# Kernel tuning notes

Measured on AMD Instinct MI355X. Metric: run time of the kernel, lower is better.

## Reference

```python
import jax, jax.numpy as jnp
import numpy as np
import math

B, T, IN_DIM = 4, 1024, 64
D, H, L, DFF = 1024, 16, 4, 4096
N_STEPS = 24
MAXLEN = 2048
DK = D // H


def _pos_encoding(max_len, d):
    pos = np.arange(max_len, dtype=np.float32)[:, None]
    div = np.exp(np.arange(0, d, 2, dtype=np.float32) * (-math.log(10000.0) / d))
    pe = np.zeros((max_len, d), dtype=np.float32)
    pe[:, 0::2] = np.sin(pos * div)
    pe[:, 1::2] = np.cos(pos * div)
    return jnp.asarray(pe)

_PE = _pos_encoding(MAXLEN, D)


def _lin(x, W, b):
    # torch Linear convention: W is (out, in)
    return x @ W.T + b


def _mha(q, kv, Wq, bq, Wk, bk, Wv, bv, Wo, bo):
    Bq, Tq, _ = q.shape
    Tk = kv.shape[1]
    Qh = _lin(q, Wq, bq).reshape(Bq, Tq, H, DK).transpose(0, 2, 1, 3)
    Kh = _lin(kv, Wk, bk).reshape(Bq, Tk, H, DK).transpose(0, 2, 1, 3)
    Vh = _lin(kv, Wv, bv).reshape(Bq, Tk, H, DK).transpose(0, 2, 1, 3)
    scores = jnp.einsum('bhqd,bhkd->bhqk', Qh, Kh) / math.sqrt(DK)
    probs = jax.nn.softmax(scores, axis=-1)
    out = jnp.einsum('bhqk,bhkd->bhqd', probs, Vh)
    out = out.transpose(0, 2, 1, 3).reshape(Bq, Tq, D)
    return _lin(out, Wo, bo)


def _ffn(x, W1, b1, W2, b2):
    return _lin(jax.nn.relu(_lin(x, W1, b1)), W2, b2)


def _ln(x, g, b, eps=1e-5):
    mu = jnp.mean(x, axis=-1, keepdims=True)
    var = jnp.var(x, axis=-1, keepdims=True)
    return (x - mu) / jnp.sqrt(var + eps) * g + b


def setup_inputs() -> dict:
    key = jax.random.key(0)
    ks = iter(jax.random.split(key, 64))
    def w(shape, s=0.02):
        return jax.random.normal(next(ks), shape, jnp.float32) * s
    inp = {'x': jax.random.normal(next(ks), (B, T, IN_DIM), jnp.float32)}
    inp['in_W'] = w((D, IN_DIM)); inp['in_b'] = jnp.zeros((D,), jnp.float32)
    for p in ['enc', 'dec']:
        for n in ['Wq', 'Wk', 'Wv', 'Wo']:
            inp[f'{p}_{n}'] = w((L, D, D))
            inp[f'{p}_b{n[1].lower()}'] = jnp.zeros((L, D), jnp.float32)
    for p in ['ffe', 'ffd']:
        inp[f'{p}_W1'] = w((DFF, D)); inp[f'{p}_b1'] = jnp.zeros((DFF,), jnp.float32)
        inp[f'{p}_W2'] = w((D, DFF)); inp[f'{p}_b2'] = jnp.zeros((D,), jnp.float32)
    for p in ['ne', 'nd']:
        inp[f'{p}_g'] = jnp.ones((D,), jnp.float32); inp[f'{p}_b'] = jnp.zeros((D,), jnp.float32)
    inp['out_W'] = w((1, D)); inp['out_b'] = jnp.zeros((1,), jnp.float32)
    inp['temb_W'] = w((D, 1)); inp['temb_b'] = jnp.zeros((D,), jnp.float32)
    return inp


def reference(x, in_W, in_b,
              enc_Wq, enc_bq, enc_Wk, enc_bk, enc_Wv, enc_bv, enc_Wo, enc_bo,
              ffe_W1, ffe_b1, ffe_W2, ffe_b2, ne_g, ne_b,
              dec_Wq, dec_bq, dec_Wk, dec_bk, dec_Wv, dec_bv, dec_Wo, dec_bo,
              ffd_W1, ffd_b1, ffd_W2, ffd_b2, nd_g, nd_b,
              out_W, out_b, temb_W, temb_b):
    batch, seq, _ = x.shape
    h = _lin(x, in_W, in_b) + _PE[:seq]
    for l in range(L):
        h = _mha(h, h, enc_Wq[l], enc_bq[l], enc_Wk[l], enc_bk[l],
                 enc_Wv[l], enc_bv[l], enc_Wo[l], enc_bo[l])
        h = _ln(h + _ffn(h, ffe_W1, ffe_b1, ffe_W2, ffe_b2), ne_g, ne_b)
    dec = jnp.zeros((batch, 1, D), x.dtype)
    preds = []
    for _ in range(N_STEPS):
        d = dec + _PE[:dec.shape[1]]
        for l in range(L):
            # same layer weights used for self- and cross-attention, as in source
            d = _mha(d, d, dec_Wq[l], dec_bq[l], dec_Wk[l], dec_bk[l],
                     dec_Wv[l], dec_bv[l], dec_Wo[l], dec_bo[l])
            d = _mha(d, h, dec_Wq[l], dec_bq[l], dec_Wk[l], dec_bk[l],
                     dec_Wv[l], dec_bv[l], dec_Wo[l], dec_bo[l])
            d = _ln(d + _ffn(d, ffd_W1, ffd_b1, ffd_W2, ffd_b2), nd_g, nd_b)
        step = _lin(d[:, -1, :], out_W, out_b)        # (B, 1)
        preds.append(step[:, None, :])                 # (B, 1, 1)
        emb = _lin(step, temb_W, temb_b)[:, None, :]   # (B, 1, D)
        dec = jnp.concatenate([dec, emb], axis=1)
    return jnp.concatenate(preds, axis=1)              # (B, n_steps, 1)
```

## Files before the change

kernel.cpp:

```cpp
#include <hip/hip_runtime.h>
#include <math.h>

#define DM    1024
#define NH    16
#define DKH   64
#define NL    4
#define DFFN  4096
#define BB    4
#define TT    1024
#define NSTEP 24
#define BT    (BB*TT)
#define MD    (BB*NSTEP)
#define CSPLIT 8
#define CKEYS  (TT/CSPLIT)
#define PSTRIDE ((size_t)MD*DM)
#define PSTRIDE_F ((size_t)MD*DFFN)

typedef __attribute__((ext_vector_type(8))) short s16x8;
typedef __attribute__((ext_vector_type(4))) short s16x4;
typedef __attribute__((ext_vector_type(4))) float f32x4;

__device__ inline short f2b(float f){
  unsigned u = __float_as_uint(f);
  u += 0x7fffu + ((u>>16)&1u);
  return (short)(u>>16);
}
__device__ inline float b2f(short h){
  return __uint_as_float(((unsigned)(unsigned short)h)<<16);
}

__device__ inline float wave_sum(float v){
  #pragma unroll
  for (int off=1; off<64; off<<=1) v += __shfl_xor(v, off, 64);
  return v;
}

__global__ __launch_bounds__(256)
void split_kernel(const float* __restrict__ X, short* __restrict__ Hi,
                  short* __restrict__ Lo, int n8)
{
  const size_t i = (size_t)blockIdx.x*256 + threadIdx.x;
  if (i >= (size_t)n8) return;
  const float4 v0 = *(const float4*)(X + i*8);
  const float4 v1 = *(const float4*)(X + i*8 + 4);
  const float f[8] = {v0.x,v0.y,v0.z,v0.w,v1.x,v1.y,v1.z,v1.w};
  s16x8 hv, lv;
  #pragma unroll
  for (int e=0;e<8;e++){
    const short h = f2b(f[e]);
    hv[e] = h;
    lv[e] = f2b(f[e] - b2f(h));
  }
  *(s16x8*)(Hi + i*8) = hv;
  *(s16x8*)(Lo + i*8) = lv;
}

__global__ void zero_kernel(float* __restrict__ p, int n) {
  int i = blockIdx.x*256 + threadIdx.x;
  if (i < n) p[i] = 0.f;
}

__global__ __launch_bounds__(256)
void k_transpose(const float* __restrict__ A, float* __restrict__ At)
{
  __shared__ float tile[32][33];
  const int bx = blockIdx.x & 31, by = blockIdx.x >> 5;
  const int x0 = bx*32, y0 = by*32;
  const int tid = threadIdx.x;
  for (int i=tid; i<1024; i+=256){
    const int r = i>>5, c = i&31;
    tile[r][c] = A[(size_t)(y0+r)*DM + x0+c];
  }
  __syncthreads();
  for (int i=tid; i<1024; i+=256){
    const int r = i>>5, c = i&31;
    At[(size_t)(x0+r)*DM + y0+c] = tile[c][r];
  }
}

__global__ __launch_bounds__(256)
void k_bc(const float* __restrict__ Wq, const float* __restrict__ bo,
          const float* __restrict__ bq, float* __restrict__ bc)
{
  const int row = blockIdx.x, tid = threadIdx.x;
  float s = 0.f;
  for (int j=tid; j<DM; j+=256) s += Wq[(size_t)row*DM + j]*bo[j];
  s = wave_sum(s);
// ... 73 lines not shown
    for (int j=0;j<4;j++){
      bh[j] = *(const s16x8*)&lB[0][wc*64+j*16+fr][fq*8];
      bl[j] = *(const s16x8*)&lB[1][wc*64+j*16+fr][fq*8];
    }
    #pragma unroll
    for (int i=0;i<4;i++)
      #pragma unroll
      for (int j=0;j<4;j++){
        acc[i][j] = __builtin_amdgcn_mfma_f32_16x16x32_bf16(ah[i], bh[j], acc[i][j], 0,0,0);
        acc[i][j] = __builtin_amdgcn_mfma_f32_16x16x32_bf16(ah[i], bl[j], acc[i][j], 0,0,0);
        acc[i][j] = __builtin_amdgcn_mfma_f32_16x16x32_bf16(al[i], bh[j], acc[i][j], 0,0,0);
      }
  }
  #pragma unroll
  for (int j=0;j<4;j++){
    const int col = n0 + wc*64 + j*16 + fr;
    const float bv = bias[col];
    #pragma unroll
    for (int i=0;i<4;i++){
      const int row0 = m0 + wr*64 + i*16 + fq*4;
      #pragma unroll
      for (int r=0;r<4;r++){
        float v = acc[i][j][r] + bv;
        if (ACT==1) v = fmaxf(v, 0.f);
        const size_t idx = (size_t)(row0+r)*N + col;
        if (OUT_MODE==0 || OUT_MODE==2) C[idx] = v;
        if (OUT_MODE==1 || OUT_MODE==2){
          const short hb = f2b(v);
          Chi[idx] = hb;
          Clo[idx] = f2b(v - b2f(hb));
        }
        if (OUT_MODE==3) Chi[idx] = f2b(v);
      }
    }
  }
}

__global__ __launch_bounds__(256)
void attn_enc(const float* __restrict__ Qg, const float* __restrict__ Kg,
              const float* __restrict__ Vg, short* __restrict__ Ohi,
              short* __restrict__ Olo)
{
  const int bh = blockIdx.y;
  const int b = bh >> 4, hh = bh & 15;
  const int row = blockIdx.x*256 + threadIdx.x;
  const size_t base = ((size_t)b*TT)*DM + hh*DKH;
  float q[64];
  {
    const float* qp = Qg + base + (size_t)row*DM;
    #pragma unroll
    for (int d4=0; d4<16; d4++){
      const float4 v = *(const float4*)(qp + d4*4);
      q[d4*4+0]=v.x; q[d4*4+1]=v.y; q[d4*4+2]=v.z; q[d4*4+3]=v.w;
    }
  }
  float o[64];
  #pragma unroll
  for (int d=0;d<64;d++) o[d]=0.f;
  float m = -INFINITY, l = 0.f;
  __shared__ float Ks[64][68];
  __shared__ float Vs[64][68];
  for (int kt=0; kt<TT; kt+=64) {
    __syncthreads();
    #pragma unroll
    for (int t=0;t<4;t++){
      const int fi = threadIdx.x + t*256;
// ... 51 lines not shown
  const float4 a = *(const float4*)(X + row*DM + tid*4);
  const float4 b = *(const float4*)(Y + row*DM + tid*4);
  const float v0=a.x+b.x, v1=a.y+b.y, v2=a.z+b.z, v3=a.w+b.w;
  float s = v0+v1+v2+v3;
  float q = v0*v0+v1*v1+v2*v2+v3*v3;
  s = wave_sum(s); q = wave_sum(q);
  __shared__ float rs[4], rq[4];
  if ((tid&63)==0){ rs[tid>>6]=s; rq[tid>>6]=q; }
  __syncthreads();
  const float S = rs[0]+rs[1]+rs[2]+rs[3];
  const float Q = rq[0]+rq[1]+rq[2]+rq[3];
  const float mean = S * (1.f/DM);
  const float var  = Q * (1.f/DM) - mean*mean;
  const float rstd = rsqrtf(var + 1e-5f);
  const float4 gv = *(const float4*)(g  + tid*4);
  const float4 bv = *(const float4*)(be + tid*4);
  const float v[4] = {(v0-mean)*rstd*gv.x + bv.x, (v1-mean)*rstd*gv.y + bv.y,
                      (v2-mean)*rstd*gv.z + bv.z, (v3-mean)*rstd*gv.w + bv.w};
  s16x4 hv, lv;
  #pragma unroll
  for (int e=0;e<4;e++){
    const short hb = f2b(v[e]);
    hv[e] = hb;
    lv[e] = f2b(v[e] - b2f(hb));
  }
  *(s16x4*)(Ohi + row*DM + tid*4) = hv;
  *(s16x4*)(Olo + row*DM + tid*4) = lv;
}


template<int MR>
__global__ __launch_bounds__(256)
void gemm_dec(const short* __restrict__ Ahi, const short* __restrict__ Alo,
              const short* __restrict__ B0hi, const short* __restrict__ B0lo,
              const short* __restrict__ B1hi, const short* __restrict__ B1lo,
              const short* __restrict__ B2hi, const short* __restrict__ B2lo,
              float* __restrict__ part, int N, int K, int KS)
{
  const short* Bhi = (blockIdx.z==0) ? B0hi : (blockIdx.z==1 ? B1hi : B2hi);
  const short* Blo = (blockIdx.z==0) ? B0lo : (blockIdx.z==1 ? B1lo : B2lo);
  float* P = part + ((size_t)blockIdx.z*KS + blockIdx.y)*(size_t)MD*N;
  const int KK = K / KS;
  const int kbase = blockIdx.y * KK;
  const int n0 = blockIdx.x * 128;
  __shared__ __align__(16) short lA[2][96][40];
  __shared__ __align__(16) short lB[2][128][40];
  const int tid = threadIdx.x;
  const int lane = tid & 63, w = tid >> 6;
  const int fr = lane & 15, fq = lane >> 4;
  constexpr int CH = MR*128;

  f32x4 acc[MR][2];
  #pragma unroll
  for (int i=0;i<MR;i++){ acc[i][0]=(f32x4){0,0,0,0}; acc[i][1]=(f32x4){0,0,0,0}; }

  for (int k0 = kbase; k0 < kbase + KK; k0 += 32) {
    __syncthreads();
    #pragma unroll
    for (int t=0; t<(CH+255)/256; t++){
      const int cc = tid + t*256;
      if (cc < CH){
        const int row = cc>>3, hl = (cc>>2)&1, kq = cc&3;
        const short* src = hl ? Alo : Ahi;
        *(s16x8*)&lA[hl][row][kq*8] = *(const s16x8*)(src + (size_t)row*K + k0 + kq*8);
      }
    }
    #pragma unroll
    for (int t=0; t<4; t++){
      const int cc = tid + t*256;
      const int row = cc>>3, hl = (cc>>2)&1, kq = cc&3;
      const short* src = hl ? Blo : Bhi;
      *(s16x8*)&lB[hl][row][kq*8] = *(const s16x8*)(src + (size_t)(n0+row)*K + k0 + kq*8);
    }
    __syncthreads();
    s16x8 bh[2], bl[2];
    #pragma unroll
    for (int j=0;j<2;j++){
      bh[j] = *(const s16x8*)&lB[0][w*32+j*16+fr][fq*8];
      bl[j] = *(const s16x8*)&lB[1][w*32+j*16+fr][fq*8];
    }
    #pragma unroll
    for (int i=0;i<MR;i++){
      const s16x8 ah = *(const s16x8*)&lA[0][i*16+fr][fq*8];
      const s16x8 al = *(const s16x8*)&lA[1][i*16+fr][fq*8];
      #pragma unroll
      for (int j=0;j<2;j++){
        acc[i][j] = __builtin_amdgcn_mfma_f32_16x16x32_bf16(ah, bh[j], acc[i][j], 0,0,0);
        acc[i][j] = __builtin_amdgcn_mfma_f32_16x16x32_bf16(ah, bl[j], acc[i][j], 0,0,0);
        acc[i][j] = __builtin_amdgcn_mfma_f32_16x16x32_bf16(al, bh[j], acc[i][j], 0,0,0);
      }
    }
  }
  #pragma unroll
  for (int j=0;j<2;j++){
    const int col = n0 + w*32 + j*16 + fr;
    #pragma unroll
    for (int i=0;i<MR;i++){
      const int row0 = i*16 + fq*4;
      #pragma unroll
      for (int r=0;r<4;r++)
        P[(size_t)(row0+r)*N + col] = acc[i][j][r];
    }
  }
}

template<int MR, int AACT>
__global__ __launch_bounds__(256)
void gemm_dec_r(const float* __restrict__ PA, const float* __restrict__ biasA,
                const short* __restrict__ Bhi, const short* __restrict__ Blo,
                float* __restrict__ part, int N, int K, int KS)
{
  float* P = part + (size_t)blockIdx.y*(size_t)MD*N;
  const int KK = K / KS;
  const int kbase = blockIdx.y * KK;
  const int n0 = blockIdx.x * 128;
  __shared__ __align__(16) short lA[2][96][40];
  __shared__ __align__(16) short lB[2][128][40];
  const int tid = threadIdx.x;
  const int lane = tid & 63, w = tid >> 6;
  const int fr = lane & 15, fq = lane >> 4;
  constexpr int CH = MR*128;
  const size_t psA = (size_t)MD*K;

  f32x4 acc[MR][2];
  #pragma unroll
  for (int i=0;i<MR;i++){ acc[i][0]=(f32x4){0,0,0,0}; acc[i][1]=(f32x4){0,0,0,0}; }

  for (int k0 = kbase; k0 < kbase + KK; k0 += 32) {
    __syncthreads();
    #pragma unroll
    for (int t=0; t<(CH+255)/256; t++){
      const int cc = tid + t*256;
      if (cc < CH){
        const int row = cc>>3, q = cc&7;
        const int k = k0 + q*4;
        float4 a = *(const float4*)(biasA + k);
        const float* src = PA + (size_t)row*K + k;
        #pragma unroll
        for (int p=0;p<8;p++){
          const float4 v = *(const float4*)(src + (size_t)p*psA);
          a.x+=v.x; a.y+=v.y; a.z+=v.z; a.w+=v.w;
        }
        if (AACT){
          a.x=fmaxf(a.x,0.f); a.y=fmaxf(a.y,0.f);
          a.z=fmaxf(a.z,0.f); a.w=fmaxf(a.w,0.f);
        }
        const float vv[4] = {a.x,a.y,a.z,a.w};
        s16x4 hv, lv;
        #pragma unroll
        for (int e=0;e<4;e++){
          const short hb = f2b(vv[e]);
          hv[e] = hb;
          lv[e] = f2b(vv[e] - b2f(hb));
        }
        *(s16x4*)&lA[0][row][q*4] = hv;
        *(s16x4*)&lA[1][row][q*4] = lv;
      }
    }
    #pragma unroll
    for (int t=0; t<4; t++){
      const int cc = tid + t*256;
      const int row = cc>>3, hl = (cc>>2)&1, kq = cc&3;
      const short* src = hl ? Blo : Bhi;
      *(s16x8*)&lB[hl][row][kq*8] = *(const s16x8*)(src + (size_t)(n0+row)*K + k0 + kq*8);
    }
    __syncthreads();
    s16x8 bh[2], bl[2];
    #pragma unroll
    for (int j=0;j<2;j++){
      bh[j] = *(const s16x8*)&lB[0][w*32+j*16+fr][fq*8];
      bl[j] = *(const s16x8*)&lB[1][w*32+j*16+fr][fq*8];
    }
    #pragma unroll
    for (int i=0;i<MR;i++){
      const s16x8 ah = *(const s16x8*)&lA[0][i*16+fr][fq*8];
      const s16x8 al = *(const s16x8*)&lA[1][i*16+fr][fq*8];
      #pragma unroll
      for (int j=0;j<2;j++){
        acc[i][j] = __builtin_amdgcn_mfma_f32_16x16x32_bf16(ah, bh[j], acc[i][j], 0,0,0);
        acc[i][j] = __builtin_amdgcn_mfma_f32_16x16x32_bf16(ah, bl[j], acc[i][j], 0,0,0);
        acc[i][j] = __builtin_amdgcn_mfma_f32_16x16x32_bf16(al, bh[j], acc[i][j], 0,0,0);
      }
    }
  }
  #pragma unroll
  for (int j=0;j<2;j++){
    const int col = n0 + w*32 + j*16 + fr;
    #pragma unroll
    for (int i=0;i<MR;i++){
      const int row0 = i*16 + fq*4;
      #pragma unroll
      for (int r=0;r<4;r++)
        P[(size_t)(row0+r)*N + col] = acc[i][j][r];
    }
  }
}

__global__ __launch_bounds__(256)
void attn_qkv(const float* __restrict__ part,
              const float* __restrict__ lbq, const float* __restrict__ lbk,
              const float* __restrict__ lbv,
              short* __restrict__ Ohi, short* __restrict__ Olo, int n)
{
  const int bh = blockIdx.x, b = bh >> 4, hh = bh & 15;
  const size_t obase = (size_t)b*DM + hh*DKH;
  __shared__ float Qs[NSTEP][68], Ks[NSTEP][68], Vs[NSTEP][68];
  __shared__ float P[NSTEP][28];
  const int tid = threadIdx.x;
  for (int t = tid; t < 3*n*16; t += 256){
    const int tensor = t / (n*16);
    const int fi = t - tensor*(n*16);
    const int row = fi >> 4, q4 = fi & 15;
    const int col0 = hh*DKH + q4*4;
    const float* bias = (tensor==0?lbq:(tensor==1?lbk:lbv));
// ... 74 lines not shown
  __syncthreads();
  for (int idx=tid; idx<n*128; idx+=256){
    const int i = idx >> 7, j = idx & 127;
    float s0=0.f,s1=0.f,s2=0.f,s3=0.f;
    #pragma unroll
    for (int d=0; d<64; d+=4){
      s0 = fmaf(Qs[i][d+0], b2f(KVs[j][d+0]), s0);
      s1 = fmaf(Qs[i][d+1], b2f(KVs[j][d+1]), s1);
      s2 = fmaf(Qs[i][d+2], b2f(KVs[j][d+2]), s2);
      s3 = fmaf(Qs[i][d+3], b2f(KVs[j][d+3]), s3);
    }
    S[i][j] = ((s0+s1)+(s2+s3))*0.125f;
  }
  __syncthreads();
  for (int t=tid; t<CKEYS*8; t+=256){
    const int row = t>>3, d8 = t&7;
    *(s16x8*)&KVs[row][d8*8] = *(const s16x8*)(Vc + kbase + (size_t)row*DM + d8*8);
  }
  if (tid < n){
    float mm=-INFINITY;
    for (int j=0;j<CKEYS;j++) mm = fmaxf(mm, S[tid][j]);
    float l=0.f;
    for (int j=0;j<CKEYS;j++){ const float p=__expf(S[tid][j]-mm); S[tid][j]=p; l+=p; }
    mlpart[((size_t)bh*CSPLIT+ks)*(2*NSTEP) + tid*2+0] = mm;
    mlpart[((size_t)bh*CSPLIT+ks)*(2*NSTEP) + tid*2+1] = l;
  }
  __syncthreads();
  for (int idx=tid; idx<n*64; idx+=256){
    const int i = idx >> 6, d = idx & 63;
    float s=0.f;
    for (int j=0;j<CKEYS;j++) s = fmaf(S[i][j], b2f(KVs[j][d]), s);
    opart[(((size_t)bh*CSPLIT+ks)*NSTEP + i)*DKH + d] = s;
  }
}

__global__ __launch_bounds__(256)
void attn_cross_comb(const float* __restrict__ opart, const float* __restrict__ mlpart,
                     short* __restrict__ Ohi, short* __restrict__ Olo, int n)
{
  const int bh = blockIdx.x;
  const int idx = blockIdx.y*256 + threadIdx.x;
  const int i = idx >> 6, d = idx & 63;
  if (i >= n) return;
  float M = -INFINITY;
  #pragma unroll
  for (int s=0;s<CSPLIT;s++)
    M = fmaxf(M, mlpart[((size_t)bh*CSPLIT+s)*(2*NSTEP) + i*2]);
  float acc = 0.f, L = 0.f;
  #pragma unroll
  for (int s=0;s<CSPLIT;s++){
    const float mm = mlpart[((size_t)bh*CSPLIT+s)*(2*NSTEP) + i*2+0];
    const float ll = mlpart[((size_t)bh*CSPLIT+s)*(2*NSTEP) + i*2+1];
    const float f = __expf(mm - M);
    acc = fmaf(f, opart[(((size_t)bh*CSPLIT+s)*NSTEP + i)*DKH + d], acc);
    L   = fmaf(f, ll, L);
  }
  const int b = bh >> 4, hh = bh & 15;
  const float v = acc / L;
  const short hb = f2b(v);
  const size_t o = ((size_t)(i*4+b))*DM + hh*DKH + d;
  Ohi[o] = hb;
  Olo[o] = f2b(v - b2f(hb));
}

__global__ __launch_bounds__(256)
void k_lnr(const float* __restrict__ partF, const float* __restrict__ fb2,
           const float* __restrict__ partR, const float* __restrict__ lbo,
           const float* __restrict__ g, const float* __restrict__ be,
           float* __restrict__ Outf, short* __restrict__ Ohi, short* __restrict__ Olo)
{
  const int row = blockIdx.x;
  __shared__ float rs[4], rq[4];
  const int tid = threadIdx.x;
  float a0,a1,a2,a3;
  {
    const float4 bv = *(const float4*)(fb2 + tid*4);
    a0=bv.x; a1=bv.y; a2=bv.z; a3=bv.w;
  }
  #pragma unroll
  for (int ks=0; ks<16; ks++){
    const float4 p = *(const float4*)(partF + (size_t)ks*PSTRIDE + (size_t)row*DM + tid*4);
    a0+=p.x; a1+=p.y; a2+=p.z; a3+=p.w;
  }
  float r0,r1,r2,r3;
  {
    const float4 bv = *(const float4*)(lbo + tid*4);
    r0=bv.x; r1=bv.y; r2=bv.z; r3=bv.w;
  }
  #pragma unroll
  for (int ks=0; ks<8; ks++){
    const float4 p = *(const float4*)(partR + (size_t)ks*PSTRIDE + (size_t)row*DM + tid*4);
    r0+=p.x; r1+=p.y; r2+=p.z; r3+=p.w;
  }
  const float v0=a0+r0, v1=a1+r1, v2=a2+r2, v3=a3+r3;
  float s = v0+v1+v2+v3;
// ... 149 lines not shown
  short* hnlo = allocS((size_t)BT*DM);
  float* t4   = alloc((size_t)BT*DM);
  float* partA = t4;
  short* fmhi = (short*)t0;
  short* fmlo = fmhi + (size_t)BT*DFFN;
  short* kcb  = allocS((size_t)NL*BT*DM);
  short* vcb  = allocS((size_t)NL*BT*DM);
  short* xshi = allocS((size_t)BT*64);
  short* xslo = allocS((size_t)BT*64);
  short* iwhi = allocS((size_t)DM*64);
  short* iwlo = allocS((size_t)DM*64);
  short* w0hi = allocS((size_t)DM*DM); short* w0lo = allocS((size_t)DM*DM);
  short* w1hi = allocS((size_t)DM*DM); short* w1lo = allocS((size_t)DM*DM);
  short* w2hi = allocS((size_t)DM*DM); short* w2lo = allocS((size_t)DM*DM);
  short* w3hi = allocS((size_t)DM*DM); short* w3lo = allocS((size_t)DM*DM);
  short* wfhi = allocS((size_t)DFFN*DM); short* wflo = allocS((size_t)DFFN*DM);
  short* wf2hi= allocS((size_t)DM*DFFN); short* wf2lo= allocS((size_t)DM*DFFN);
  float* bqo  = alloc((size_t)NL*DM);
  float* zbuf = alloc((size_t)DM);
  float* dbuf = alloc((size_t)MD*DM);
  short* dphi = allocS((size_t)MD*DM);  short* dplo = allocS((size_t)MD*DM);
  short* dlhi = allocS((size_t)MD*DM);  short* dllo = allocS((size_t)MD*DM);
  short* dahi = allocS((size_t)MD*DM);  short* dalo = allocS((size_t)MD*DM);
  float* partB = alloc((size_t)16*MD*DM);
  float* partC = alloc((size_t)8*MD*DM);
  float* opart= alloc((size_t)BB*NH*CSPLIT*NSTEP*DKH);
  float* mlp  = alloc((size_t)BB*NH*CSPLIT*2*NSTEP);

  const size_t MM = (size_t)DM*DM;
  short* dwq = (short*)t0;
  short* dwk = (short*)t1;
  short* dwv = (short*)t2;
  short* dwo = (short*)h;
  short* fw1h = t3hi; short* fw1l = t3lo;
  short* fw2h = hnhi; short* fw2l = hnlo;
  short* wch  = hshi; short* wcl  = hslo;
  float* wotf = t4;
  float* wcf  = t4 + MM;

  auto cvt = [&](const float* src, short* hi, short* lo, size_t n){
    split_kernel<<<(int)((n/8 + 255)/256), 256, 0, stream>>>(src, hi, lo, (int)(n/8));
  };

  cvt(x,    xshi, xslo, (size_t)BT*64);
  cvt(in_W, iwhi, iwlo, (size_t)DM*64);
  cvt(ffe_W1, wfhi,  wflo,  (size_t)DFFN*DM);
  cvt(ffe_W2, wf2hi, wf2lo, (size_t)DM*DFFN);
  zero_kernel<<<(DM+255)/256, 256, 0, stream>>>(zbuf, DM);

  gemm_split<0,0><<<dim3(BT/128, DM/128), 256, 0, stream>>>(
      xshi, xslo, iwhi, iwlo, in_b, h, (short*)nullptr, (short*)nullptr, BT, DM, 64);
  add_pe_split<<<BT, 256, 0, stream>>>(h, hshi, hslo);

  for (int l=0; l<NL; ++l) {
    const size_t wo = (size_t)l*DM*DM, bo_ = (size_t)l*DM;
    cvt(enc_Wq+wo, w0hi, w0lo, MM);
    cvt(enc_Wk+wo, w1hi, w1lo, MM);
    cvt(enc_Wv+wo, w2hi, w2lo, MM);
    cvt(enc_Wo+wo, w3hi, w3lo, MM);
    gemm_split<0,0><<<dim3(32,8),256,0,stream>>>(hshi, hslo, w0hi, w0lo, enc_bq+bo_,
        t0, (short*)nullptr, (short*)nullptr, BT, DM, DM);
    gemm_split<0,0><<<dim3(32,8),256,0,stream>>>(hshi, hslo, w1hi, w1lo, enc_bk+bo_,
        t1, (short*)nullptr, (short*)nullptr, BT, DM, DM);
    gemm_split<0,0><<<dim3(32,8),256,0,stream>>>(hshi, hslo, w2hi, w2lo, enc_bv+bo_,
        t2, (short*)nullptr, (short*)nullptr, BT, DM, DM);
    attn_enc<<<dim3(TT/256, BB*NH),256,0,stream>>>(t0, t1, t2, t3hi, t3lo);
    gemm_split<0,2><<<dim3(32,8),256,0,stream>>>(t3hi, t3lo, w3hi, w3lo, enc_bo+bo_,
        hn, hnhi, hnlo, BT, DM, DM);
    gemm_split<1,1><<<dim3(32,32),256,0,stream>>>(hnhi, hnlo, wfhi, wflo, ffe_b1,
        (float*)nullptr, fmhi, fmlo, BT, DFFN, DM);
    gemm_split<0,0><<<dim3(32,8),256,0,stream>>>(fmhi, fmlo, wf2hi, wf2lo, ffe_b2,
        t4, (short*)nullptr, (short*)nullptr, BT, DM, DFFN);
    ln_add_split<<<BT,256,0,stream>>>(hn, t4, ne_g, ne_b, hshi, hslo);
  }

  for (int l=0; l<NL; ++l) {
    const size_t wo = (size_t)l*DM*DM, bo_ = (size_t)l*DM;
    cvt(dec_Wk+wo, w0hi, w0lo, MM);
    cvt(dec_Wv+wo, w1hi, w1lo, MM);
    gemm_split<0,3><<<dim3(32,8),256,0,stream>>>(hshi, hslo, w0hi, w0lo, dec_bk+bo_,
        (float*)nullptr, kcb+(size_t)l*BT*DM, (short*)nullptr, BT, DM, DM);
    gemm_split<0,3><<<dim3(32,8),256,0,stream>>>(hshi, hslo, w1hi, w1lo, dec_bv+bo_,
        (float*)nullptr, vcb+(size_t)l*BT*DM, (short*)nullptr, BT, DM, DM);
  }

  for (int l=0; l<NL; ++l) {
    const size_t wo = (size_t)l*DM*DM;
    cvt(dec_Wq+wo, dwq + (size_t)l*2*MM, dwq + (size_t)l*2*MM + MM, MM);
    cvt(dec_Wk+wo, dwk + (size_t)l*2*MM, dwk + (size_t)l*2*MM + MM, MM);
    cvt(dec_Wv+wo, dwv + (size_t)l*2*MM, dwv + (size_t)l*2*MM + MM, MM);
    cvt(dec_Wo+wo, dwo + (size_t)l*2*MM, dwo + (size_t)l*2*MM + MM, MM);
  }
  cvt(ffd_W1, fw1h, fw1l, (size_t)DFFN*DM);
  cvt(ffd_W2, fw2h, fw2l, (size_t)DM*DFFN);
  for (int l=0; l<NL; ++l) {
    const size_t wo = (size_t)l*DM*DM, bo_ = (size_t)l*DM;
    k_transpose<<<1024, 256, 0, stream>>>(dec_Wo+wo, wotf);
    cvt(wotf,      w0hi, w0lo, MM);
    cvt(dec_Wq+wo, w1hi, w1lo, MM);
    gemm_split<0,0><<<dim3(8,8),256,0,stream>>>(w1hi, w1lo, w0hi, w0lo, zbuf,
        wcf, (short*)nullptr, (short*)nullptr, DM, DM, DM);
    k_bc<<<DM, 256, 0, stream>>>(dec_Wq+wo, dec_bo+bo_, dec_bq+bo_, bqo+bo_);
    cvt(wcf, wch + (size_t)l*MM, wcl + (size_t)l*MM, MM);
  }

  #define GD(MRv, grid, ...) do { switch(MRv){ \
    case 1: gemm_dec<1><<<grid,256,0,stream>>>(__VA_ARGS__); break; \
    case 2: gemm_dec<2><<<grid,256,0,stream>>>(__VA_ARGS__); break; \
    case 3: gemm_dec<3><<<grid,256,0,stream>>>(__VA_ARGS__); break; \
    case 4: gemm_dec<4><<<grid,256,0,stream>>>(__VA_ARGS__); break; \
    case 5: gemm_dec<5><<<grid,256,0,stream>>>(__VA_ARGS__); break; \
    default: gemm_dec<6><<<grid,256,0,stream>>>(__VA_ARGS__); break; } } while(0)
  #define GDR(MRv, AACT, grid, ...) do { switch(MRv){ \
    case 1: gemm_dec_r<1,AACT><<<grid,256,0,stream>>>(__VA_ARGS__); break; \
    case 2: gemm_dec_r<2,AACT><<<grid,256,0,stream>>>(__VA_ARGS__); break; \
    case 3: gemm_dec_r<3,AACT><<<grid,256,0,stream>>>(__VA_ARGS__); break; \
    case 4: gemm_dec_r<4,AACT><<<grid,256,0,stream>>>(__VA_ARGS__); break; \
    case 5: gemm_dec_r<5,AACT><<<grid,256,0,stream>>>(__VA_ARGS__); break; \
    default: gemm_dec_r<6,AACT><<<grid,256,0,stream>>>(__VA_ARGS__); break; } } while(0)

  k_init0<<<BB, 256, 0, stream>>>(dphi, dplo);
  for (int s=0; s<NSTEP; ++s){
    const int n = s+1, rows = 4*n;
    const int Mt = (rows + 15) & ~15;
    const int MR = Mt >> 4;
    for (int l=0; l<NL; ++l){
      const short* qh = dwq + (size_t)l*2*MM; const short* ql = qh + MM;
      const short* kh = dwk + (size_t)l*2*MM; const short* kl = kh + MM;
      const short* vh = dwv + (size_t)l*2*MM; const short* vl = vh + MM;
      const short* oh = dwo + (size_t)l*2*MM; const short* ol = oh + MM;
      const short* ch = wch + (size_t)l*MM;   const short* cl = wcl + (size_t)l*MM;
      const float* lbq = dec_bq + (size_t)l*DM;
      const float* lbk = dec_bk + (size_t)l*DM;
      const float* lbv = dec_bv + (size_t)l*DM;
      const float* lbo = dec_bo + (size_t)l*DM;
      const float* lbc = bqo + (size_t)l*DM;
      const short* in_hi = (l==0) ? dphi : dlhi;
      const short* in_lo = (l==0) ? dplo : dllo;
      GD(MR, dim3(8,8,3), in_hi,in_lo, qh,ql, kh,kl, vh,vl, partA, DM, DM, 8);
      attn_qkv<<<BB*NH,256,0,stream>>>(partA, lbq, lbk, lbv, dahi, dalo, n);
      GD(MR, dim3(8,8,1), dahi,dalo, ch,cl, ch,cl, ch,cl, partB, DM, DM, 8);
      attn_cross_part<<<dim3(CSPLIT, BB*NH),256,0,stream>>>(partB, lbc,
          kcb + (size_t)l*BT*DM, vcb + (size_t)l*BT*DM, opart, mlp, n);
      attn_cross_comb<<<dim3(BB*NH, 6),256,0,stream>>>(opart, mlp, dahi, dalo, n);
      GD(MR, dim3(8,8,1), dahi,dalo, oh,ol, oh,ol, oh,ol, partC, DM, DM, 8);
      GDR(MR, 0, dim3(32,8), partC, lbo, fw1h, fw1l, partA, DFFN, DM, 8);
      GDR(MR, 1, dim3(8,16), partA, ffd_b1, fw2h, fw2l, partB, DM, DFFN, 16);
      k_lnr<<<rows,256,0,stream>>>(partB, ffd_b2, partC, lbo, nd_g, nd_b,
          dbuf, dlhi, dllo);
    }
    k_out<<<BB, 256, 0, stream>>>(dbuf, out_W, out_b, temb_W, temb_b, dout,
        dphi, dplo, s);
  }
  #undef GD
  #undef GDR
}
```

Baseline: 13.22 ms.

## Use single-bf16 decoder weights, fuse cross-attn combine into Wo GEMM, batch encoder QKV

Decoder weights are now stored as a single bf16 copy instead of a hi/lo split. This halves weight traffic in the decoder GEMMs and drops one of the three MFMAs per tile. The cross-attention split-softmax combine is folded into the A-tile load of the output-projection GEMM, which removes a kernel launch and an intermediate buffer. The encoder Q/K/V projections are batched into one grid-z launch, and the weight conversion kernels are merged. The cost is lower precision on decoder weights, where the lo-part correction is dropped, and repeated combine work across N-blocks.

```diff
diff --git a/kernel.cpp b/kernel.cpp
--- a/kernel.cpp
+++ b/kernel.cpp
@@ -14,7 +14,6 @@
 #define CSPLIT 8
 #define CKEYS  (TT/CSPLIT)
 #define PSTRIDE ((size_t)MD*DM)
-#define PSTRIDE_F ((size_t)MD*DFFN)
 
 typedef __attribute__((ext_vector_type(8))) short s16x8;
 typedef __attribute__((ext_vector_type(4))) short s16x4;
@@ -53,6 +52,48 @@
   }
   *(s16x8*)(Hi + i*8) = hv;
   *(s16x8*)(Lo + i*8) = lv;
+}
+
+__global__ __launch_bounds__(256)
+void split4_kernel(const float* __restrict__ X0, const float* __restrict__ X1,
+                   const float* __restrict__ X2, const float* __restrict__ X3,
+                   short* __restrict__ H0, short* __restrict__ L0,
+                   short* __restrict__ H1, short* __restrict__ L1,
+                   short* __restrict__ H2, short* __restrict__ L2,
+                   short* __restrict__ H3, short* __restrict__ L3, int n8)
+{
+  const size_t i = (size_t)blockIdx.x*256 + threadIdx.x;
+  if (i >= (size_t)n8) return;
+  const int z = blockIdx.y;
+  const float* X = (z==0)?X0:(z==1?X1:(z==2?X2:X3));
+  short* Hi = (z==0)?H0:(z==1?H1:(z==2?H2:H3));
+  short* Lo = (z==0)?L0:(z==1?L1:(z==2?L2:L3));
+  const float4 v0 = *(const float4*)(X + i*8);
+  const float4 v1 = *(const float4*)(X + i*8 + 4);
+  const float f[8] = {v0.x,v0.y,v0.z,v0.w,v1.x,v1.y,v1.z,v1.w};
+  s16x8 hv, lv;
+  #pragma unroll
+  for (int e=0;e<8;e++){
+    const short h = f2b(f[e]);
+    hv[e] = h;
+    lv[e] = f2b(f[e] - b2f(h));
+  }
+  *(s16x8*)(Hi + i*8) = hv;
+  *(s16x8*)(Lo + i*8) = lv;
+}
+
+__global__ __launch_bounds__(256)
+void cvt_b(const float* __restrict__ X, short* __restrict__ O, int n8)
+{
+  const size_t i = (size_t)blockIdx.x*256 + threadIdx.x;
+  if (i >= (size_t)n8) return;
+  const float4 v0 = *(const float4*)(X + i*8);
+  const float4 v1 = *(const float4*)(X + i*8 + 4);
+  const float f[8] = {v0.x,v0.y,v0.z,v0.w,v1.x,v1.y,v1.z,v1.w};
+  s16x8 hv;
+  #pragma unroll
+  for (int e=0;e<8;e++) hv[e] = f2b(f[e]);
+  *(s16x8*)(O + i*8) = hv;
 }
 
 __global__ void zero_kernel(float* __restrict__ p, int n) {
@@ -192,6 +233,83 @@
         }
         if (OUT_MODE==3) Chi[idx] = f2b(v);
       }
+    }
+  }
+}
+
+__global__ __launch_bounds__(256, 2)
+void gemm_split_qkv(const short* __restrict__ Ahi, const short* __restrict__ Alo,
+                const short* __restrict__ B0h, const short* __restrict__ B0l,
+                const short* __restrict__ B1h, const short* __restrict__ B1l,
+                const short* __restrict__ B2h, const short* __restrict__ B2l,
+                const float* __restrict__ b0, const float* __restrict__ b1,
+                const float* __restrict__ b2,
+                float* __restrict__ C0, float* __restrict__ C1, float* __restrict__ C2,
+                int M, int N, int K)
+{
+  const int z = blockIdx.z;
+  const short* Bhi = (z==0)?B0h:(z==1?B1h:B2h);
+  const short* Blo = (z==0)?B0l:(z==1?B1l:B2l);
+  const float* bias = (z==0)?b0:(z==1?b1:b2);
+  float* C = (z==0)?C0:(z==1?C1:C2);
+  __shared__ __align__(16) short lA[2][128][40];
+  __shared__ __align__(16) short lB[2][128][40];
+  const int tid = threadIdx.x;
+  const int m0 = blockIdx.x*128, n0 = blockIdx.y*128;
+  const int lane = tid & 63, w = tid >> 6;
+  const int wr = w >> 1, wc = w & 1;
+  const int fr = lane & 15, fq = lane >> 4;
+
+  f32x4 acc[4][4];
+  #pragma unroll
+  for (int i=0;i<4;i++)
+    #pragma unroll
+    for (int j=0;j<4;j++) acc[i][j] = (f32x4){0.f,0.f,0.f,0.f};
+
+  for (int k0 = 0; k0 < K; k0 += 32) {
+    __syncthreads();
+    #pragma unroll
+    for (int j=0;j<2;j++){
+      const int cc = tid + j*256;
+      const int row = cc >> 2, kq = cc & 3;
+      const size_t ga = (size_t)(m0+row)*K + k0 + kq*8;
+      const size_t gb = (size_t)(n0+row)*K + k0 + kq*8;
+      *(s16x8*)&lA[0][row][kq*8] = *(const s16x8*)(Ahi + ga);
+      *(s16x8*)&lA[1][row][kq*8] = *(const s16x8*)(Alo + ga);
+      *(s16x8*)&lB[0][row][kq*8] = *(const s16x8*)(Bhi + gb);
+      *(s16x8*)&lB[1][row][kq*8] = *(const s16x8*)(Blo + gb);
+    }
+    __syncthreads();
+    s16x8 ah[4], al[4], bh[4], bl[4];
+    #pragma unroll
+    for (int i=0;i<4;i++){
+      ah[i] = *(const s16x8*)&lA[0][wr*64+i*16+fr][fq*8];
+      al[i] = *(const s16x8*)&lA[1][wr*64+i*16+fr][fq*8];
+    }
+    #pragma unroll
+    for (int j=0;j<4;j++){
+      bh[j] = *(const s16x8*)&lB[0][wc*64+j*16+fr][fq*8];
+      bl[j] = *(const s16x8*)&lB[1][wc*64+j*16+fr][fq*8];
+    }
+    #pragma unroll
+    for (int i=0;i<4;i++)
+      #pragma unroll
+      for (int j=0;j<4;j++){
+        acc[i][j] = __builtin_amdgcn_mfma_f32_16x16x32_bf16(ah[i], bh[j], acc[i][j], 0,0,0);
+        acc[i][j] = __builtin_amdgcn_mfma_f32_16x16x32_bf16(ah[i], bl[j], acc[i][j], 0,0,0);
+        acc[i][j] = __builtin_amdgcn_mfma_f32_16x16x32_bf16(al[i], bh[j], acc[i][j], 0,0,0);
+      }
+  }
+  #pragma unroll
+  for (int j=0;j<4;j++){
+    const int col = n0 + wc*64 + j*16 + fr;
+    const float bv = bias[col];
+    #pragma unroll
+    for (int i=0;i<4;i++){
+      const int row0 = m0 + wr*64 + i*16 + fq*4;
+      #pragma unroll
+      for (int r=0;r<4;r++)
+        C[(size_t)(row0+r)*N + col] = acc[i][j][r] + bv;
     }
   }
 }
@@ -309,19 +427,17 @@
 template<int MR>
 __global__ __launch_bounds__(256)
 void gemm_dec(const short* __restrict__ Ahi, const short* __restrict__ Alo,
-              const short* __restrict__ B0hi, const short* __restrict__ B0lo,
-              const short* __restrict__ B1hi, const short* __restrict__ B1lo,
-              const short* __restrict__ B2hi, const short* __restrict__ B2lo,
+              const short* __restrict__ B0, const short* __restrict__ B1,
+              const short* __restrict__ B2,
               float* __restrict__ part, int N, int K, int KS)
 {
-  const short* Bhi = (blockIdx.z==0) ? B0hi : (blockIdx.z==1 ? B1hi : B2hi);
-  const short* Blo = (blockIdx.z==0) ? B0lo : (blockIdx.z==1 ? B1lo : B2lo);
+  const short* B = (blockIdx.z==0) ? B0 : (blockIdx.z==1 ? B1 : B2);
   float* P = part + ((size_t)blockIdx.z*KS + blockIdx.y)*(size_t)MD*N;
   const int KK = K / KS;
   const int kbase = blockIdx.y * KK;
   const int n0 = blockIdx.x * 128;
   __shared__ __align__(16) short lA[2][96][40];
-  __shared__ __align__(16) short lB[2][128][40];
+  __shared__ __align__(16) short lB[128][40];
   const int tid = threadIdx.x;
   const int lane = tid & 63, w = tid >> 6;
   const int fr = lane & 15, fq = lane >> 4;
@@ -343,28 +459,23 @@
       }
     }
     #pragma unroll
-    for (int t=0; t<4; t++){
+    for (int t=0; t<2; t++){
       const int cc = tid + t*256;
-      const int row = cc>>3, hl = (cc>>2)&1, kq = cc&3;
-      const short* src = hl ? Blo : Bhi;
-      *(s16x8*)&lB[hl][row][kq*8] = *(const s16x8*)(src + (size_t)(n0+row)*K + k0 + kq*8);
+      const int row = cc>>2, kq = cc&3;
+      *(s16x8*)&lB[row][kq*8] = *(const s16x8*)(B + (size_t)(n0+row)*K + k0 + kq*8);
     }
     __syncthreads();
-    s16x8 bh[2], bl[2];
-    #pragma unroll
-    for (int j=0;j<2;j++){
-      bh[j] = *(const s16x8*)&lB[0][w*32+j*16+fr][fq*8];
-      bl[j] = *(const s16x8*)&lB[1][w*32+j*16+fr][fq*8];
-    }
+    s16x8 bq[2];
+    #pragma unroll
+    for (int j=0;j<2;j++) bq[j] = *(const s16x8*)&lB[w*32+j*16+fr][fq*8];
     #pragma unroll
     for (int i=0;i<MR;i++){
       const s16x8 ah = *(const s16x8*)&lA[0][i*16+fr][fq*8];
       const s16x8 al = *(const s16x8*)&lA[1][i*16+fr][fq*8];
       #pragma unroll
       for (int j=0;j<2;j++){
-        acc[i][j] = __builtin_amdgcn_mfma_f32_16x16x32_bf16(ah, bh[j], acc[i][j], 0,0,0);
-        acc[i][j] = __builtin_amdgcn_mfma_f32_16x16x32_bf16(ah, bl[j], acc[i][j], 0,0,0);
-        acc[i][j] = __builtin_amdgcn_mfma_f32_16x16x32_bf16(al, bh[j], acc[i][j], 0,0,0);
+        acc[i][j] = __builtin_amdgcn_mfma_f32_16x16x32_bf16(ah, bq[j], acc[i][j], 0,0,0);
+        acc[i][j] = __builtin_amdgcn_mfma_f32_16x16x32_bf16(al, bq[j], acc[i][j], 0,0,0);
       }
     }
   }
@@ -384,7 +495,7 @@
 template<int MR, int AACT>
 __global__ __launch_bounds__(256)
 void gemm_dec_r(const float* __restrict__ PA, const float* __restrict__ biasA,
-                const short* __restrict__ Bhi, const short* __restrict__ Blo,
+                const short* __restrict__ B,
                 float* __restrict__ part, int N, int K, int KS)
 {
   float* P = part + (size_t)blockIdx.y*(size_t)MD*N;
@@ -392,7 +503,7 @@
   const int kbase = blockIdx.y * KK;
   const int n0 = blockIdx.x * 128;
   __shared__ __align__(16) short lA[2][96][40];
-  __shared__ __align__(16) short lB[2][128][40];
+  __shared__ __align__(16) short lB[128][40];
   const int tid = threadIdx.x;
   const int lane = tid & 63, w = tid >> 6;
   const int fr = lane & 15, fq = lane >> 4;
@@ -435,28 +546,123 @@
       }
     }
     #pragma unroll
-    for (int t=0; t<4; t++){
+    for (int t=0; t<2; t++){
       const int cc = tid + t*256;
-      const int row = cc>>3, hl = (cc>>2)&1, kq = cc&3;
-      const short* src = hl ? Blo : Bhi;
-      *(s16x8*)&lB[hl][row][kq*8] = *(const s16x8*)(src + (size_t)(n0+row)*K + k0 + kq*8);
+      const int row = cc>>2, kq = cc&3;
+      *(s16x8*)&lB[row][kq*8] = *(const s16x8*)(B + (size_t)(n0+row)*K + k0 + kq*8);
     }
     __syncthreads();
-    s16x8 bh[2], bl[2];
-    #pragma unroll
-    for (int j=0;j<2;j++){
-      bh[j] = *(const s16x8*)&lB[0][w*32+j*16+fr][fq*8];
-      bl[j] = *(const s16x8*)&lB[1][w*32+j*16+fr][fq*8];
-    }
+    s16x8 bq[2];
+    #pragma unroll
+    for (int j=0;j<2;j++) bq[j] = *(const s16x8*)&lB[w*32+j*16+fr][fq*8];
     #pragma unroll
     for (int i=0;i<MR;i++){
       const s16x8 ah = *(const s16x8*)&lA[0][i*16+fr][fq*8];
       const s16x8 al = *(const s16x8*)&lA[1][i*16+fr][fq*8];
       #pragma unroll
       for (int j=0;j<2;j++){
-        acc[i][j] = __builtin_amdgcn_mfma_f32_16x16x32_bf16(ah, bh[j], acc[i][j], 0,0,0);
-        acc[i][j] = __builtin_amdgcn_mfma_f32_16x16x32_bf16(ah, bl[j], acc[i][j], 0,0,0);
-        acc[i][j] = __builtin_amdgcn_mfma_f32_16x16x32_bf16(al, bh[j], acc[i][j], 0,0,0);
+        acc[i][j] = __builtin_amdgcn_mfma_f32_16x16x32_bf16(ah, bq[j], acc[i][j], 0,0,0);
+        acc[i][j] = __builtin_amdgcn_mfma_f32_16x16x32_bf16(al, bq[j], acc[i][j], 0,0,0);
+      }
+    }
+  }
+  #pragma unroll
+  for (int j=0;j<2;j++){
+    const int col = n0 + w*32 + j*16 + fr;
+    #pragma unroll
+    for (int i=0;i<MR;i++){
+      const int row0 = i*16 + fq*4;
+      #pragma unroll
+      for (int r=0;r<4;r++)
+        P[(size_t)(row0+r)*N + col] = acc[i][j][r];
+    }
+  }
+}
+
+template<int MR>
+__global__ __launch_bounds__(256)
+void gemm_dec_c(const float* __restrict__ opart, const float* __restrict__ mlp,
+                const short* __restrict__ B,
+                float* __restrict__ part, int N, int K, int KS, int n)
+{
+  float* P = part + (size_t)blockIdx.y*(size_t)MD*N;
+  const int KK = K / KS;
+  const int kbase = blockIdx.y * KK;
+  const int n0 = blockIdx.x * 128;
+  __shared__ __align__(16) short lA[2][96][40];
+  __shared__ __align__(16) short lB[128][40];
+  const int tid = threadIdx.x;
+  const int lane = tid & 63, w = tid >> 6;
+  const int fr = lane & 15, fq = lane >> 4;
+  constexpr int CH = MR*128;
+
+  f32x4 acc[MR][2];
+  #pragma unroll
+  for (int i=0;i<MR;i++){ acc[i][0]=(f32x4){0,0,0,0}; acc[i][1]=(f32x4){0,0,0,0}; }
+
+  for (int k0 = kbase; k0 < kbase + KK; k0 += 32) {
+    __syncthreads();
+    const int hh = k0 >> 6;
+    #pragma unroll
+    for (int t=0; t<(CH+255)/256; t++){
+      const int cc = tid + t*256;
+      if (cc < CH){
+        const int row = cc>>3, q = cc&7;
+        const int d = (k0 & 63) + q*4;
+        const int b = row & 3, i = row >> 2;
+        const int bh = b*16 + hh;
+        float4 a = {0.f,0.f,0.f,0.f};
+        if (i < n){
+          const float* ml = mlp + (size_t)bh*CSPLIT*(2*NSTEP) + i*2;
+          float M = -INFINITY;
+          #pragma unroll
+          for (int s=0;s<CSPLIT;s++)
+            M = fmaxf(M, ml[(size_t)s*(2*NSTEP)]);
+          float L = 0.f;
+          #pragma unroll
+          for (int s=0;s<CSPLIT;s++){
+            const float mm = ml[(size_t)s*(2*NSTEP)];
+            const float ll = ml[(size_t)s*(2*NSTEP) + 1];
+            const float f = __expf(mm - M);
+            const float4 v = *(const float4*)(opart +
+                (((size_t)(bh*CSPLIT+s)*NSTEP + i)*DKH + d));
+            a.x = fmaf(f, v.x, a.x); a.y = fmaf(f, v.y, a.y);
+            a.z = fmaf(f, v.z, a.z); a.w = fmaf(f, v.w, a.w);
+            L = fmaf(f, ll, L);
+          }
+          const float inv = 1.f / L;
+          a.x*=inv; a.y*=inv; a.z*=inv; a.w*=inv;
+        }
+        const float vv[4] = {a.x,a.y,a.z,a.w};
+        s16x4 hv, lv;
+        #pragma unroll
+        for (int e=0;e<4;e++){
+          const short hb = f2b(vv[e]);
+          hv[e] = hb;
+          lv[e] = f2b(vv[e] - b2f(hb));
+        }
+        *(s16x4*)&lA[0][row][q*4] = hv;
+        *(s16x4*)&lA[1][row][q*4] = lv;
+      }
+    }
+    #pragma unroll
+    for (int t=0; t<2; t++){
+      const int cc = tid + t*256;
+      const int row = cc>>2, kq = cc&3;
+      *(s16x8*)&lB[row][kq*8] = *(const s16x8*)(B + (size_t)(n0+row)*K + k0 + kq*8);
+    }
+    __syncthreads();
+    s16x8 bq[2];
+    #pragma unroll
+    for (int j=0;j<2;j++) bq[j] = *(const s16x8*)&lB[w*32+j*16+fr][fq*8];
+    #pragma unroll
+    for (int i=0;i<MR;i++){
+      const s16x8 ah = *(const s16x8*)&lA[0][i*16+fr][fq*8];
+      const s16x8 al = *(const s16x8*)&lA[1][i*16+fr][fq*8];
+      #pragma unroll
+      for (int j=0;j<2;j++){
+        acc[i][j] = __builtin_amdgcn_mfma_f32_16x16x32_bf16(ah, bq[j], acc[i][j], 0,0,0);
+        acc[i][j] = __builtin_amdgcn_mfma_f32_16x16x32_bf16(al, bq[j], acc[i][j], 0,0,0);
       }
     }
   }
@@ -597,35 +803,6 @@
     for (int j=0;j<CKEYS;j++) s = fmaf(S[i][j], b2f(KVs[j][d]), s);
     opart[(((size_t)bh*CSPLIT+ks)*NSTEP + i)*DKH + d] = s;
   }
-}
-
-__global__ __launch_bounds__(256)
-void attn_cross_comb(const float* __restrict__ opart, const float* __restrict__ mlpart,
-                     short* __restrict__ Ohi, short* __restrict__ Olo, int n)
-{
-  const int bh = blockIdx.x;
-  const int idx = blockIdx.y*256 + threadIdx.x;
-  const int i = idx >> 6, d = idx & 63;
-  if (i >= n) return;
-  float M = -INFINITY;
-  #pragma unroll
-  for (int s=0;s<CSPLIT;s++)
-    M = fmaxf(M, mlpart[((size_t)bh*CSPLIT+s)*(2*NSTEP) + i*2]);
-  float acc = 0.f, L = 0.f;
-  #pragma unroll
-  for (int s=0;s<CSPLIT;s++){
-    const float mm = mlpart[((size_t)bh*CSPLIT+s)*(2*NSTEP) + i*2+0];
-    const float ll = mlpart[((size_t)bh*CSPLIT+s)*(2*NSTEP) + i*2+1];
-    const float f = __expf(mm - M);
-    acc = fmaf(f, opart[(((size_t)bh*CSPLIT+s)*NSTEP + i)*DKH + d], acc);
-    L   = fmaf(f, ll, L);
-  }
-  const int b = bh >> 4, hh = bh & 15;
-  const float v = acc / L;
-  const short hb = f2b(v);
-  const size_t o = ((size_t)(i*4+b))*DM + hh*DKH + d;
-  Ohi[o] = hb;
-  Olo[o] = f2b(v - b2f(hb));
 }
 
 __global__ __launch_bounds__(256)
@@ -841,14 +1018,17 @@
   short* dwk = (short*)t1;
   short* dwv = (short*)t2;
   short* dwo = (short*)h;
-  short* fw1h = t3hi; short* fw1l = t3lo;
-  short* fw2h = hnhi; short* fw2l = hnlo;
-  short* wch  = hshi; short* wcl  = hslo;
+  short* fw1 = t3hi;
+  short* fw2 = t3lo;
+  short* wcb = hnhi;
   float* wotf = t4;
   float* wcf  = t4 + MM;
 
   auto cvt = [&](const float* src, short* hi, short* lo, size_t n){
     split_kernel<<<(int)((n/8 + 255)/256), 256, 0, stream>>>(src, hi, lo, (int)(n/8));
+  };
+  auto cvtb = [&](const float* src, short* o, size_t n){
+    cvt_b<<<(int)((n/8 + 255)/256), 256, 0, stream>>>(src, o, (int)(n/8));
   };
 
   cvt(x,    xshi, xslo, (size_t)BT*64);
@@ -863,16 +1043,12 @@
 
   for (int l=0; l<NL; ++l) {
     const size_t wo = (size_t)l*DM*DM, bo_ = (size_t)l*DM;
-    cvt(enc_Wq+wo, w0hi, w0lo, MM);
-    cvt(enc_Wk+wo, w1hi, w1lo, MM);
-    cvt(enc_Wv+wo, w2hi, w2lo, MM);
-    cvt(enc_Wo+wo, w3hi, w3lo, MM);
-    gemm_split<0,0><<<dim3(32,8),256,0,stream>>>(hshi, hslo, w0hi, w0lo, enc_bq+bo_,
-        t0, (short*)nullptr, (short*)nullptr, BT, DM, DM);
-    gemm_split<0,0><<<dim3(32,8),256,0,stream>>>(hshi, hslo, w1hi, w1lo, enc_bk+bo_,
-        t1, (short*)nullptr, (short*)nullptr, BT, DM, DM);
-    gemm_split<0,0><<<dim3(32,8),256,0,stream>>>(hshi, hslo, w2hi, w2lo, enc_bv+bo_,
-        t2, (short*)nullptr, (short*)nullptr, BT, DM, DM);
+    split4_kernel<<<dim3((int)((MM/8+255)/256), 4), 256, 0, stream>>>(
+        enc_Wq+wo, enc_Wk+wo, enc_Wv+wo, enc_Wo+wo,
+        w0hi, w0lo, w1hi, w1lo, w2hi, w2lo, w3hi, w3lo, (int)(MM/8));
+    gemm_split_qkv<<<dim3(32,8,3),256,0,stream>>>(hshi, hslo,
+        w0hi, w0lo, w1hi, w1lo, w2hi, w2lo,
+        enc_bq+bo_, enc_bk+bo_, enc_bv+bo_, t0, t1, t2, BT, DM, DM);
     attn_enc<<<dim3(TT/256, BB*NH),256,0,stream>>>(t0, t1, t2, t3hi, t3lo);
     gemm_split<0,2><<<dim3(32,8),256,0,stream>>>(t3hi, t3lo, w3hi, w3lo, enc_bo+bo_,
         hn, hnhi, hnlo, BT, DM, DM);
@@ -893,15 +1069,12 @@
         (float*)nullptr, vcb+(size_t)l*BT*DM, (short*)nullptr, BT, DM, DM);
   }
 
-  for (int l=0; l<NL; ++l) {
-    const size_t wo = (size_t)l*DM*DM;
-    cvt(dec_Wq+wo, dwq + (size_t)l*2*MM, dwq + (size_t)l*2*MM + MM, MM);
-    cvt(dec_Wk+wo, dwk + (size_t)l*2*MM, dwk + (size_t)l*2*MM + MM, MM);
-    cvt(dec_Wv+wo, dwv + (size_t)l*2*MM, dwv + (size_t)l*2*MM + MM, MM);
-    cvt(dec_Wo+wo, dwo + (size_t)l*2*MM, dwo + (size_t)l*2*MM + MM, MM);
-  }
-  cvt(ffd_W1, fw1h, fw1l, (size_t)DFFN*DM);
-  cvt(ffd_W2, fw2h, fw2l, (size_t)DM*DFFN);
+  cvtb(dec_Wq, dwq, (size_t)NL*MM);
+  cvtb(dec_Wk, dwk, (size_t)NL*MM);
+  cvtb(dec_Wv, dwv, (size_t)NL*MM);
+  cvtb(dec_Wo, dwo, (size_t)NL*MM);
+  cvtb(ffd_W1, fw1, (size_t)DFFN*DM);
+  cvtb(ffd_W2, fw2, (size_t)DM*DFFN);
   for (int l=0; l<NL; ++l) {
     const size_t wo = (size_t)l*DM*DM, bo_ = (size_t)l*DM;
     k_transpose<<<1024, 256, 0, stream>>>(dec_Wo+wo, wotf);
@@ -910,7 +1083,7 @@
     gemm_split<0,0><<<dim3(8,8),256,0,stream>>>(w1hi, w1lo, w0hi, w0lo, zbuf,
         wcf, (short*)nullptr, (short*)nullptr, DM, DM, DM);
     k_bc<<<DM, 256, 0, stream>>>(dec_Wq+wo, dec_bo+bo_, dec_bq+bo_, bqo+bo_);
-    cvt(wcf, wch + (size_t)l*MM, wcl + (size_t)l*MM, MM);
+    cvtb(wcf, wcb + (size_t)l*MM, MM);
   }
 
   #define GD(MRv, grid, ...) do { switch(MRv){ \
@@ -927,6 +1100,13 @@
     case 4: gemm_dec_r<4,AACT><<<grid,256,0,stream>>>(__VA_ARGS__); break; \
     case 5: gemm_dec_r<5,AACT><<<grid,256,0,stream>>>(__VA_ARGS__); break; \
     default: gemm_dec_r<6,AACT><<<grid,256,0,stream>>>(__VA_ARGS__); break; } } while(0)
+  #define GDC(MRv, grid, ...) do { switch(MRv){ \
+    case 1: gemm_dec_c<1><<<grid,256,0,stream>>>(__VA_ARGS__); break; \
+    case 2: gemm_dec_c<2><<<grid,256,0,stream>>>(__VA_ARGS__); break; \
+    case 3: gemm_dec_c<3><<<grid,256,0,stream>>>(__VA_ARGS__); break; \
+    case 4: gemm_dec_c<4><<<grid,256,0,stream>>>(__VA_ARGS__); break; \
+    case 5: gemm_dec_c<5><<<grid,256,0,stream>>>(__VA_ARGS__); break; \
+    default: gemm_dec_c<6><<<grid,256,0,stream>>>(__VA_ARGS__); break; } } while(0)
 
   k_init0<<<BB, 256, 0, stream>>>(dphi, dplo);
   for (int s=0; s<NSTEP; ++s){
@@ -934,11 +1114,11 @@
     const int Mt = (rows + 15) & ~15;
     const int MR = Mt >> 4;
     for (int l=0; l<NL; ++l){
-      const short* qh = dwq + (size_t)l*2*MM; const short* ql = qh + MM;
-      const short* kh = dwk + (size_t)l*2*MM; const short* kl = kh + MM;
-      const short* vh = dwv + (size_t)l*2*MM; const short* vl = vh + MM;
-      const short* oh = dwo + (size_t)l*2*MM; const short* ol = oh + MM;
-      const short* ch = wch + (size_t)l*MM;   const short* cl = wcl + (size_t)l*MM;
+      const short* qb = dwq + (size_t)l*MM;
+      const short* kb = dwk + (size_t)l*MM;
+      const short* vb = dwv + (size_t)l*MM;
+      const short* ob = dwo + (size_t)l*MM;
+      const short* cb = wcb + (size_t)l*MM;
       const float* lbq = dec_bq + (size_t)l*DM;
       const float* lbk = dec_bk + (size_t)l*DM;
       const float* lbv = dec_bv + (size_t)l*DM;
@@ -946,15 +1126,14 @@
       const float* lbc = bqo + (size_t)l*DM;
       const short* in_hi = (l==0) ? dphi : dlhi;
       const short* in_lo = (l==0) ? dplo : dllo;
-      GD(MR, dim3(8,8,3), in_hi,in_lo, qh,ql, kh,kl, vh,vl, partA, DM, DM, 8);
+      GD(MR, dim3(8,8,3), in_hi,in_lo, qb, kb, vb, partA, DM, DM, 8);
       attn_qkv<<<BB*NH,256,0,stream>>>(partA, lbq, lbk, lbv, dahi, dalo, n);
-      GD(MR, dim3(8,8,1), dahi,dalo, ch,cl, ch,cl, ch,cl, partB, DM, DM, 8);
+      GD(MR, dim3(8,8,1), dahi,dalo, cb, cb, cb, partB, DM, DM, 8);
       attn_cross_part<<<dim3(CSPLIT, BB*NH),256,0,stream>>>(partB, lbc,
           kcb + (size_t)l*BT*DM, vcb + (size_t)l*BT*DM, opart, mlp, n);
-      attn_cross_comb<<<dim3(BB*NH, 6),256,0,stream>>>(opart, mlp, dahi, dalo, n);
-      GD(MR, dim3(8,8,1), dahi,dalo, oh,ol, oh,ol, oh,ol, partC, DM, DM, 8);
-      GDR(MR, 0, dim3(32,8), partC, lbo, fw1h, fw1l, partA, DFFN, DM, 8);
-      GDR(MR, 1, dim3(8,16), partA, ffd_b1, fw2h, fw2l, partB, DM, DFFN, 16);
+      GDC(MR, dim3(8,8), opart, mlp, ob, partC, DM, DM, 8, n);
+      GDR(MR, 0, dim3(32,8), partC, lbo, fw1, partA, DFFN, DM, 8);
+      GDR(MR, 1, dim3(8,16), partA, ffd_b1, fw2, partB, DM, DFFN, 16);
       k_lnr<<<rows,256,0,stream>>>(partB, ffd_b2, partC, lbo, nd_g, nd_b,
           dbuf, dlhi, dllo);
     }
@@ -963,4 +1142,5 @@
   }
   #undef GD
   #undef GDR
-}
+  #undef GDC
+}
```

New measurement: 13.33 ms. No clear change (+0.9%).
